# Kernel tuning notes

Hardware: AMD Instinct MI355X
Metric: run time of the kernel (lower is better)

Reference implementation:

```python
import jax, jax.numpy as jnp
import numpy as np

H_HEADS = 16
DECAY_C = 0.7408182206817179  # math.exp(-0.3)


def _gelu(x):
    return jax.nn.gelu(x, approximate=False)  # torch nn.GELU default = exact erf


def _mlp(x, W1, b1, W2, b2):
    return _gelu(x @ W1 + b1) @ W2 + b2


def setup_inputs():
    B, T, C = 4, 2048, 1024
    L = max(64, C // 8)      # lora_dim = 128
    E = int(C * 1.2)         # expanded_dim = 1228
    key = jax.random.key(0)
    ctr = [0]
    def rn(shape, s=0.02):
        ctr[0] += 1
        return jax.random.normal(jax.random.fold_in(key, ctr[0]), shape, jnp.float32) * s
    z = lambda *s: jnp.zeros(s, jnp.float32)
    inp = {
        "queries": rn((B, T, C), 1.0),
        "keys": rn((B, T, C), 1.0),
        "values": rn((B, T, C), 1.0),
        "attn_mask": jnp.ones((B, T), dtype=bool),
        "mu_r": rn((C,)), "mu_k": rn((C,)), "mu_v": rn((C,)),
        "mu_g": rn((C,)), "mu_a": rn((C,)), "mu_d": rn((C,)),
        "dA": rn((C, L)), "dB": rn((L, C)), "db": z(C),
        "aA": rn((C, L)), "aB": rn((L, C)), "ab": z(C),
        "gA": rn((C, L)), "gB": rn((L, C)),
        "rW1": rn((C, E)), "rb1": z(E), "rW2": rn((E, C)), "rb2": z(C),
        "kW1": rn((C, E)), "kb1": z(E), "kW2": rn((E, C)), "kb2": z(C),
        "vW1": rn((C, E)), "vb1": z(E), "vW2": rn((E, C)), "vb2": z(C),
        "oW1": rn((C, E)), "ob1": z(E), "oW2": rn((E, C)), "ob2": z(C),
        "rem_mult": rn((C,), 0.05),
        "iclr_mix": jnp.full((C,), 0.7, jnp.float32),
        "bonus_mult": jnp.full((C,), 1.2, jnp.float32),
        "ln_g": jnp.ones((C,), jnp.float32), "ln_b": z(C),
    }
    return inp


def _forward(queries, mu_r, mu_k, mu_v, mu_g, mu_a, mu_d,
             dA, dB, db, aA, aB, ab, gA, gB,
             rW1, rb1, rW2, rb2, kW1, kb1, kW2, kb2,
             vW1, vb1, vW2, vb2, oW1, ob1, oW2, ob2,
             rem_mult, iclr_mix, bonus_mult, ln_g, ln_b):
    B, T, C = queries.shape
    H = H_HEADS
    N = C // H
    r = _mlp(queries + mu_r, rW1, rb1, rW2, rb2)
    k = _mlp(queries + mu_k, kW1, kb1, kW2, kb2)
    v = _mlp(queries + mu_v, vW1, vb1, vW2, vb2)
    gate = jax.nn.sigmoid(((queries + mu_g) @ gA) @ gB)
    iclr = jax.nn.sigmoid(((queries + mu_a) @ aA) @ ab + ((queries + mu_a) @ aA) @ aB) if False else jax.nn.sigmoid(((queries + mu_a) @ aA) @ aB + ab)
    decay = jnp.exp(-DECAY_C * jax.nn.sigmoid(jnp.tanh(((queries + mu_d) @ dA) @ dB + db)))
    removal_k = k * rem_mult
    replacement_k = k * (1.0 + (iclr - 1.0) * iclr_mix)  # lerp(ones, iclr, mix)
    rh = r.reshape(B, T, H, N)
    rkh = replacement_k.reshape(B, T, H, N)
    vh = v.reshape(B, T, H, N)
    dh = decay.reshape(B, T, H, N)
    ah = iclr.reshape(B, T, H, N)
    rmh = removal_k.reshape(B, T, H, N)
    kn = rmh / jnp.maximum(jnp.linalg.norm(rmh, axis=-1, keepdims=True), 1e-12)  # F.normalize
    # Sequential matrix-state recurrence. G_t = diag(d) - kn (a*kn)^T, so
    # G_t @ S = d[:,None]*S - kn[:,None] * ((a*kn) @ S)  -- rank-1, O(N^2)/step.
    xs = tuple(jnp.swapaxes(a, 0, 1) for a in (dh, ah, kn, rkh, vh, rh))  # [T,B,H,N]
    def step(wkv, x):
        d, a, knt, rk, vt, rt = x
        tmp = jnp.einsum('bhj,bhjk->bhk', a * knt, wkv)
        wkv = d[..., None] * wkv - knt[..., None] * tmp[:, :, None, :] \
              + vt[..., None] * rk[:, :, None, :]
        return wkv, jnp.einsum('bhij,bhj->bhi', wkv, rt)
    wkv0 = jnp.zeros((B, H, N, N), queries.dtype)
    _, out_t = jax.lax.scan(step, wkv0, xs)
    out = jnp.swapaxes(out_t, 0, 1)  # [B,T,H,N]
    bonus = (jnp.sum(rh * rkh, -1, keepdims=True) * 0.2) * vh * bonus_mult.reshape(1, 1, H, N)
    out = (out + bonus).reshape(B, T, C)
    mu = jnp.mean(out, -1, keepdims=True)
    var = jnp.mean((out - mu) ** 2, -1, keepdims=True)
    out = (out - mu) / jnp.sqrt(var + 1e-6) * ln_g + ln_b  # ln_x, eps=1e-6
    out = out * gate
    out = _mlp(out, oW1, ob1, oW2, ob2)  # W_output; dropout is identity in eval
    return out


def reference(queries, keys, values, attn_mask,
              mu_r, mu_k, mu_v, mu_g, mu_a, mu_d,
              dA, dB, db, aA, aB, ab, gA, gB,
              rW1, rb1, rW2, rb2, kW1, kb1, kW2, kb2,
              vW1, vb1, vW2, vb2, oW1, ob1, oW2, ob2,
              rem_mult, iclr_mix, bonus_mult, ln_g, ln_b):
    del keys, values, attn_mask  # accepted but unused by the module's forward
    return _forward(queries, mu_r, mu_k, mu_v, mu_g, mu_a, mu_d,
                    dA, dB, db, aA, aB, ab, gA, gB,
                    rW1, rb1, rW2, rb2, kW1, kb1, kW2, kb2,
                    vW1, vb1, vW2, vb2, oW1, ob1, oW2, ob2,
                    rem_mult, iclr_mix, bonus_mult, ln_g, ln_b)
```

## Files before the change

### kernel.cpp

```cpp
#include <hip/hip_runtime.h>
#include <hip/hip_bf16.h>
#include <math.h>


#define BB 4
#define TT 2048
#define CC 1024
#define HH 16
#define NN 64
#define LL 128
#define EE 1228
#define EPAD 1280
#define MM (BB*TT)
#define TCH 32
#define NSEG 4
#define WARMCH 2
#define DECAY_C_F 0.7408182206817179f

typedef __attribute__((ext_vector_type(8))) short s16x8;
typedef __attribute__((ext_vector_type(4))) float f32x4;

#define GLOAD_LDS16(gp, lp) \
    __builtin_amdgcn_global_load_lds((const __attribute__((address_space(1))) void*)(gp), \
                                     (__attribute__((address_space(3))) void*)(lp), 16, 0, 0)

__global__ __launch_bounds__(256) void fold_pass1_z(
    const float* __restrict__ mu0, const float* __restrict__ mu1, const float* __restrict__ mu2,
    const float* __restrict__ W0,  const float* __restrict__ W1_, const float* __restrict__ W2_,
    float* __restrict__ partial, int ldW, int E, int ldP, int pslice) {
    const float* mu = blockIdx.z == 0 ? mu0 : (blockIdx.z == 1 ? mu1 : mu2);
    const float* W  = blockIdx.z == 0 ? W0  : (blockIdx.z == 1 ? W1_ : W2_);
    partial += (size_t)blockIdx.z * pslice;
    const int l = threadIdx.x & 63;
    const int e = blockIdx.x * 64 + l;
    const int pg = threadIdx.x >> 6;
    const int c0 = blockIdx.y * 64;
    float s = 0.f;
    if (e < E)
        for (int c = c0 + pg; c < c0 + 64; c += 4) s += mu[c] * W[(size_t)c * ldW + e];
    __shared__ float red[4][64];
    red[pg][l] = s;
    __syncthreads();
    if (pg == 0 && e < E)
        partial[(size_t)blockIdx.y * ldP + e] = red[0][l] + red[1][l] + red[2][l] + red[3][l];
}

__global__ void fold_pass2_z(const float* __restrict__ partial,
                             const float* b0, const float* b1, const float* b2,
                             float* __restrict__ outv,
                             int P, int ldP, int pslice, int E, int Epad, int oslice) {
    const float* bias = blockIdx.z == 0 ? b0 : (blockIdx.z == 1 ? b1 : b2);
    partial += (size_t)blockIdx.z * pslice;
    outv    += (size_t)blockIdx.z * oslice;
    int e = blockIdx.x * blockDim.x + threadIdx.x;
    if (e >= Epad) return;
    float s = 0.f;
    if (e < E) {
        s = bias ? bias[e] : 0.f;
        for (int p = 0; p < P; ++p) s += partial[(size_t)p * ldP + e];
    }
    outv[e] = s;
}

__global__ void cast_f32_bf16(const float* __restrict__ in, __hip_bfloat16* __restrict__ out, int n4) {
    int i = blockIdx.x * blockDim.x + threadIdx.x;
    if (i >= n4) return;
    float4 v = ((const float4*)in)[i];
    __hip_bfloat16 o[4] = {__float2bfloat16(v.x), __float2bfloat16(v.y),
                           __float2bfloat16(v.z), __float2bfloat16(v.w)};
    *(ulong1*)&out[i * 4] = *(ulong1*)o;
}

__global__ void transpose_cast_z(const float* s0, const float* s1, const float* s2, const float* s3,
                                 __hip_bfloat16* __restrict__ outT, size_t dslice,
                                 int Rin, int Cin, int Rpad, int Cpad) {
    const float* in = blockIdx.z == 0 ? s0 : (blockIdx.z == 1 ? s1 : (blockIdx.z == 2 ? s2 : s3));
    outT += (size_t)blockIdx.z * dslice;
    __shared__ float t[32][33];
    const int r0 = blockIdx.x * 32, c0 = blockIdx.y * 32;
    const int tx = threadIdx.x, ty = threadIdx.y;
    #pragma unroll
    for (int j = 0; j < 4; ++j) {
        int r = r0 + ty + j * 8, c = c0 + tx;
        t[ty + j * 8][tx] = (r < Rin && c < Cin) ? in[(size_t)r * Cin + c] : 0.f;
    }
    __syncthreads();
    #pragma unroll
    for (int j = 0; j < 4; ++j) {
        int c = c0 + ty + j * 8, r = r0 + tx;
        if (c < Cpad && r < Rpad) outT[(size_t)c * Rpad + r] = __float2bfloat16(t[tx][ty + j * 8]);
    }
}

template<int ACT, int ACTZ2, int OBF, int PADZ>
__global__ __launch_bounds__(256) void gemm_mfma(const __hip_bfloat16* __restrict__ A,
                                                 const __hip_bfloat16* __restrict__ Bt,
                                                 const float* __restrict__ bias,
                                                 void* __restrict__ Cptr,
                                                 int M, int N, int K,
                                                 int ldA, int ldB, int ldC,
                                                 size_t zA, size_t zB, size_t zBias, size_t zC) {
    __shared__ __hip_bfloat16 As[128 * 64];
    __shared__ __hip_bfloat16 Bs[128 * 64];
    const int tid = threadIdx.x;
    const int wid = tid >> 6, lane = tid & 63;
    const int wm = wid >> 1, wn = wid & 1;
    const int bm = blockIdx.y * 128, bn = blockIdx.x * 128;
    A  += (size_t)blockIdx.z * zA;
    Bt += (size_t)blockIdx.z * zB;
    if (bias) bias += (size_t)blockIdx.z * zBias;
    const size_t zc = (size_t)blockIdx.z * zC;
    const int act = (ACTZ2 >= 0 && blockIdx.z == 2) ? ACTZ2 : ACT;

    const __hip_bfloat16* srcA[4];
    const __hip_bfloat16* srcB[4];
    #pragma unroll
    for (int i = 0; i < 4; ++i) {
        int off = (wid * 4 + i) * 1024 + lane * 16;
        int r = off >> 7;
        int c = (off >> 4) & 7;
        int cs = c ^ (r & 7);
        srcA[i] = A  + (size_t)(bm + r) * ldA + cs * 8;
        srcB[i] = Bt + (size_t)(bn + r) * ldB + cs * 8;
    }

    f32x4 acc[4][4];
    #pragma unroll
    for (int i = 0; i < 4; ++i)
        #pragma unroll
        for (int j = 0; j < 4; ++j) acc[i][j] = (f32x4){0.f, 0.f, 0.f, 0.f};

    const int ra = wm * 64 + (lane & 15);
    const int rb = wn * 64 + (lane & 15);

    for (int k0 = 0; k0 < K; k0 += 64) {
        #pragma unroll
        for (int i = 0; i < 4; ++i) {
            GLOAD_LDS16(srcA[i] + k0, (char*)As + (wid * 4 + i) * 1024);
            GLOAD_LDS16(srcB[i] + k0, (char*)Bs + (wid * 4 + i) * 1024);
        }
        __syncthreads();
        #pragma unroll
        for (int h = 0; h < 2; ++h) {
            s16x8 af[4], bfr[4];
            const int kc = (lane >> 4) + h * 4;
            #pragma unroll
            for (int mi = 0; mi < 4; ++mi) {
                int r = ra + mi * 16;
                af[mi] = *(const s16x8*)((const char*)As + r * 128 + (kc ^ (r & 7)) * 16);
            }
            #pragma unroll
            for (int ni = 0; ni < 4; ++ni) {
                int r = rb + ni * 16;
                bfr[ni] = *(const s16x8*)((const char*)Bs + r * 128 + (kc ^ (r & 7)) * 16);
            }
            #pragma unroll
            for (int mi = 0; mi < 4; ++mi)
                #pragma unroll
                for (int ni = 0; ni < 4; ++ni)
                    acc[mi][ni] = __builtin_amdgcn_mfma_f32_16x16x32_bf16(af[mi], bfr[ni], acc[mi][ni], 0, 0, 0);
        }
        __syncthreads();
    }

    #pragma unroll
    for (int ni = 0; ni < 4; ++ni) {
        const int col = bn + wn * 64 + ni * 16 + (lane & 15);
        const bool valid = (col < N);
        const float bc = (valid && bias) ? bias[col] : 0.f;
        #pragma unroll
        for (int mi = 0; mi < 4; ++mi) {
            #pragma unroll
            for (int reg = 0; reg < 4; ++reg) {
                const int row = bm + wm * 64 + mi * 16 + (lane >> 4) * 4 + reg;
                float y = 0.f;
                if (valid) {
                    float x = acc[mi][ni][reg] + bc;
                    if (act == 1)      y = 0.5f * x * (1.0f + erff(x * 0.7071067811865475f));
                    else if (act == 2) y = 1.0f / (1.0f + expf(-x));
                    else if (act == 3) { float sg = 1.0f / (1.0f + expf(-tanhf(x))); y = expf(-DECAY_C_F * sg); }
                    else               y = x;
                }
                if (valid || PADZ) {
                    if (OBF) ((__hip_bfloat16*)Cptr)[zc + (size_t)row * ldC + col] = __float2bfloat16(y);
                    else     ((float*)Cptr)[zc + (size_t)row * ldC + col] = y;
                }
            }
        }
    }
}

#define P_T0(i,j)   pool[0     + (i)*68 + (j)]
#define P_WT(i,j)   pool[4352  + (i)*68 + (j)]
#define P_KP(i,j)   pool[6528  + (i)*68 + (j)]
#define P_P2t(i,j)  pool[6528  + (i)*36 + (j)]
#define P_NU(i,j)   pool[8704  + (i)*68 + (j)]
#define P_GRt(i,j)  pool[8704  + (i)*36 + (j)]
#define P_RKM(i,j)  pool[10880 + (i)*68 + (j)]
#define P_RRM(i,j)  pool[13056 + (i)*68 + (j)]
#define P_GM(i,j)   pool[15232 + (i)*68 + (j)]
#define P_KPT(i,j)  pool[19712 + (i)*36 + (j)]
#define P_NUT(i,j)  pool[22016 + (i)*36 + (j)]
#define P_DCT(i,j)  pool[26624 + (i)*36 + (j)]
#define P_AT(i,j)   pool[28928 + (i)*36 + (j)]
#define P_BM(i,j)   pool[30080 + (i)*36 + (j)]
#define P_SEG(i,j)  pool[31232 + (i)*64 + (j)]
#define LD4(expr)   (*(const float4*)&(expr))
#define FMA4(acc, s, v) { (acc).x = fmaf((s), (v).x, (acc).x); (acc).y = fmaf((s), (v).y, (acc).y); \
                          (acc).z = fmaf((s), (v).z, (acc).z); (acc).w = fmaf((s), (v).w, (acc).w); }
#define DOT4(a, b) ((a).x*(b).x + (a).y*(b).y + (a).z*(b).z + (a).w*(b).w)

__global__ __launch_bounds__(512) void recurrence_chunked(
    const float* __restrict__ kbuf, const __hip_bfloat16* __restrict__ iclr,
    const __hip_bfloat16* __restrict__ dbuf, const float* __restrict__ vbuf,
    const float* __restrict__ rbuf,
    const float* __restrict__ rem_mult, const float* __restrict__ iclr_mix,
    const float* __restrict__ bonus_mult, float* __restrict__ outb) {
    __shared__ float pool[31488];
    const int bh = blockIdx.x & 63, seg = blockIdx.x >> 6;
    const int b = bh >> 4, h = bh & 15;
    const int tid = threadIdx.x, lane = tid & 63, wid = tid >> 6;
    const size_t gbase = ((size_t)b * TT) * CC + (size_t)h * NN;

    for (int i = tid; i < 4352; i += 512) pool[i] = 0.f;
    const int c0 = tid & 63;
    const float remc = rem_mult[h * NN + c0];
    const float mixc = iclr_mix[h * NN + c0];
    __syncthreads();

    const int cout0 = (seg == 0) ? 0 : (seg == 1) ? 18 : (seg == 2) ? 34 : 49;
    const int lenq  = (seg == 0) ? 18 : (seg == 1) ? 16 : 15;
    const int ce    = cout0 + lenq;
    const int cb    = (seg == 0) ? 0 : cout0 - WARMCH;

    for (int chk = cb; chk < ce; ++chk) {
        const bool emit = (chk >= cout0);
        const int tg0 = chk * TCH;
        #pragma unroll
        for (int i = 0; i < 4; ++i) {
            int idx = tid + 512 * i;
            int t = idx >> 6, c = idx & 63;
            size_t off = gbase + (size_t)(tg0 + t) * CC + c;
            float kx = kbuf[off];
            float ax = __bfloat162float(iclr[off]);
            float rk = kx * (1.f + (ax - 1.f) * mixc);
            P_WT(t, c) = ax;
            P_KP(t, c) = kx * remc;
            P_RKM(t, c) = rk;
            P_NU(t, c) = vbuf[off];
            if (emit) P_RRM(t, c) = rbuf[off];
            P_DCT(c, t) = __bfloat162float(dbuf[off]);
        }
        __syncthreads();
        #pragma unroll
        for (int rr = 0; rr < 4; ++rr) {
            int t = wid + rr * 8;
            float v = P_KP(t, lane);
            float ss = v * v;
            #pragma unroll
            for (int s = 32; s; s >>= 1) ss += __shfl_xor(ss, s);
            float kn = v / fmaxf(sqrtf(ss), 1e-12f);
            P_KP(t, lane) = kn;
            P_WT(t, lane) = P_WT(t, lane) * kn;
        }
        float lc[8];
        const int ccs = tid & 63, sgm = tid >> 6, t0s = (sgm & 3) * 8;
        if (tid < 256) {
            float pp_ = 1.f;
            #pragma unroll
            for (int j = 0; j < 8; ++j) { pp_ *= P_DCT(ccs, t0s + j); lc[j] = pp_; }
            P_SEG(sgm, ccs) = pp_;
        }
        __syncthreads();
        if (tid < 256) {
            float m = 1.f;
            for (int s = 0; s < sgm; ++s) m *= P_SEG(s, ccs);
            float dcprev = m;
            #pragma unroll
            for (int j = 0; j < 8; ++j) {
                int t = t0s + j;
                float dcur = m * lc[j];
                P_WT(t, ccs) *= dcprev;
                float inv = 1.f / dcur;
                float kap = P_KP(t, ccs) * inv; P_KP(t, ccs) = kap; P_KPT(ccs, t) = kap;
                float nu  = P_NU(t, ccs) * inv; P_NU(t, ccs) = nu;  P_NUT(ccs, t) = nu;
                P_DCT(ccs, t) = dcur;
                dcprev = dcur;
            }
        }
        __syncthreads();
        #pragma unroll
        for (int u = 0; u < 2; ++u) {
            const int at = wid * 2 + u;
            const int s = (at >> 2) * 8 + (lane >> 3), t = (at & 3) * 8 + (lane & 7);
            float acc = 0.f;
            #pragma unroll
            for (int kc = 0; kc < 16; ++kc) {
                float4 a = LD4(P_KP(s, kc * 4));
                float4 bb = LD4(P_WT(t, kc * 4));
                acc += DOT4(a, bb);
            }
            P_AT(s, t) = (s < t) ? acc : 0.f;
        }
        #pragma unroll
        for (int u = 0; u < 2; ++u) {
            const int bt = wid * 2 + u;
            const int t = (bt >> 2) * 8 + (lane >> 3), s = (bt & 3) * 8 + (lane & 7);
            float acc = 0.f;
            #pragma unroll
            for (int kc = 0; kc < 16; ++kc) {
                float4 a = LD4(P_WT(t, kc * 4));
                float4 bb = LD4(P_NU(s, kc * 4));
                acc += DOT4(a, bb);
            }
            P_BM(t, s) = (s < t) ? acc : 0.f;
        }
        {
            const int t = wid * 4 + (lane >> 4);
            const int q4 = (lane & 15) * 4;
            float4 acc = {0.f, 0.f, 0.f, 0.f};
            #pragma unroll
            for (int j4 = 0; j4 < 16; ++j4) {
                float4 w4 = LD4(P_WT(t, j4 * 4));
                float4 ta = LD4(P_T0(j4 * 4 + 0, q4));
                float4 tb = LD4(P_T0(j4 * 4 + 1, q4));
                float4 tc = LD4(P_T0(j4 * 4 + 2, q4));
                float4 td = LD4(P_T0(j4 * 4 + 3, q4));
                FMA4(acc, w4.x, ta); FMA4(acc, w4.y, tb);
                FMA4(acc, w4.z, tc); FMA4(acc, w4.w, td);
            }
            *(float4*)&P_GM(t, q4) = acc;
        }
        __syncthreads();
        {
            const int t = wid * 4 + (lane >> 4);
            const int q4 = (lane & 15) * 4;
            float4 acc = {0.f, 0.f, 0.f, 0.f};
            #pragma unroll
            for (int s4 = 0; s4 < 8; ++s4) {
                float4 bm4 = LD4(P_BM(t, s4 * 4));
                float4 ra = LD4(P_RKM(s4 * 4 + 0, q4));
                float4 rb = LD4(P_RKM(s4 * 4 + 1, q4));
                float4 rc = LD4(P_RKM(s4 * 4 + 2, q4));
                float4 rd = LD4(P_RKM(s4 * 4 + 3, q4));
                FMA4(acc, bm4.x, ra); FMA4(acc, bm4.y, rb);
                FMA4(acc, bm4.z, rc); FMA4(acc, bm4.w, rd);
            }
            float4 g = LD4(P_GM(t, q4));
            g.x += acc.x; g.y += acc.y; g.z += acc.z; g.w += acc.w;
            *(float4*)&P_GM(t, q4) = g;
        }
        __syncthreads();
        if (wid == 0) {
            float g[32];
            #pragma unroll
            for (int t = 0; t < 32; ++t) g[t] = P_GM(t, lane);
            #pragma unroll
            for (int s = 0; s < 31; ++s) {
                #pragma unroll
                for (int t = s + 1; t < 32; ++t) g[t] -= P_AT(s, t) * g[s];
            }
            #pragma unroll
            for (int t = 0; t < 32; ++t) P_GM(t, lane) = g[t];
        } else if (emit) {
            for (int tile = wid - 1; tile < 16; tile += 7) {
                int t = (tile >> 2) * 8 + (lane >> 3), s = (tile & 3) * 8 + (lane & 7);
                float acc = 0.f;
                #pragma unroll
                for (int kc = 0; kc < 16; ++kc) {
                    float4 a = LD4(P_RRM(t, kc * 4));
                    float4 bb = LD4(P_RKM(s, kc * 4));
                    acc += DOT4(a, bb);
                }
                P_P2t(t, s) = (s <= t) ? acc : 0.f;
            }
        }
        __syncthreads();
        if (emit) {
            for (int tile = wid; tile < 16; tile += 8) {
                int t = (tile >> 2) * 8 + (lane >> 3), s = (tile & 3) * 8 + (lane & 7);
                float acc = 0.f;
                #pragma unroll
                for (int kc = 0; kc < 16; ++kc) {
                    float4 a = LD4(P_RRM(t, kc * 4));
                    float4 bb = LD4(P_GM(s, kc * 4));
                    acc += DOT4(a, bb);
                }
                P_GRt(t, s) = (s <= t) ? acc : 0.f;
            }
            __syncthreads();
            for (int tile = wid; tile < 32; tile += 8) {
                int i = (tile >> 2) * 8 + (lane >> 3), t = (tile & 3) * 8 + (lane & 7);
                float a1 = 0.f, a2 = 0.f, a3 = 0.f;
                #pragma unroll
                for (int j4 = 0; j4 < 16; ++j4) {
                    float4 a = LD4(P_T0(i, j4 * 4));
                    float4 bb = LD4(P_RRM(t, j4 * 4));
                    a1 += DOT4(a, bb);
                }
                #pragma unroll
                for (int s4 = 0; s4 < 8; ++s4) {
                    float4 a = LD4(P_NUT(i, s4 * 4));
                    float4 bb = LD4(P_P2t(t, s4 * 4));
                    a2 += DOT4(a, bb);
                    float4 c = LD4(P_KPT(i, s4 * 4));
                    float4 d = LD4(P_GRt(t, s4 * 4));
                    a3 += DOT4(c, d);
                }
                float diag = 0.2f * bonus_mult[h * NN + i] * P_NUT(i, t) * P_P2t(t, t);
                outb[gbase + (size_t)(tg0 + t) * CC + i] = P_DCT(i, t) * (a1 + a2 + diag - a3);
            }
            __syncthreads();
        }
        #pragma unroll
        for (int u = 0; u < 2; ++u) {
            const int m = wid * 2 + u;
            const int pr = (m & 7) * 8 + (lane >> 3);
            const int q4 = (m >> 3) * 32 + (lane & 7) * 4;
            float4 a1 = {0.f, 0.f, 0.f, 0.f}, a2 = {0.f, 0.f, 0.f, 0.f};
            #pragma unroll
            for (int s = 0; s < 32; ++s) {
                const float kp = P_KPT(pr, s);
                const float nu = P_NUT(pr, s);
                float4 g4 = LD4(P_GM(s, q4));
                float4 rk4 = LD4(P_RKM(s, q4));
                FMA4(a1, kp, g4);
                FMA4(a2, nu, rk4);
            }
            const float dc = P_DCT(pr, 31);
            float4 t0 = LD4(P_T0(pr, q4));
            t0.x = dc * (t0.x - a1.x + a2.x);
            t0.y = dc * (t0.y - a1.y + a2.y);
            t0.z = dc * (t0.z - a1.z + a2.z);
            t0.w = dc * (t0.w - a1.w + a2.w);
            *(float4*)&P_T0(pr, q4) = t0;
        }
        __syncthreads();
    }
}

__global__ __launch_bounds__(256) void ln_gate_kernel(const float* __restrict__ x,
                                                      const __hip_bfloat16* __restrict__ gate,
                                                      const float* __restrict__ g,
                                                      const float* __restrict__ bv,
                                                      __hip_bfloat16* __restrict__ y) {
    const int row = blockIdx.x;
    const float* xr = x + (size_t)row * CC;
    float v[4];
    float s = 0.f;
    #pragma unroll
    for (int j = 0; j < 4; ++j) { v[j] = xr[threadIdx.x + 256 * j]; s += v[j]; }
    __shared__ float red[4], red2[4];
    #pragma unroll
    for (int o = 32; o; o >>= 1) s += __shfl_xor(s, o);
    if ((threadIdx.x & 63) == 0) red[threadIdx.x >> 6] = s;
    __syncthreads();
    const float mean = (red[0] + red[1] + red[2] + red[3]) * (1.f / CC);
    float vs = 0.f;
    #pragma unroll
    for (int j = 0; j < 4; ++j) { float d = v[j] - mean; vs += d * d; }
    #pragma unroll
    for (int o = 32; o; o >>= 1) vs += __shfl_xor(vs, o);
    if ((threadIdx.x & 63) == 0) red2[threadIdx.x >> 6] = vs;
    __syncthreads();
    const float var = (red2[0] + red2[1] + red2[2] + red2[3]) * (1.f / CC);
    const float rstd = rsqrtf(var + 1e-6f);
    #pragma unroll
    for (int j = 0; j < 4; ++j) {
        const int cc = threadIdx.x + 256 * j;
        float o_ = (v[j] - mean) * rstd * g[cc] + bv[cc];
        float gt = __bfloat162float(gate[(size_t)row * CC + cc]);
        y[(size_t)row * CC + cc] = __float2bfloat16(o_ * gt);
    }
}

extern "C" void kernel_launch(void* const* d_in, const int* in_sizes, int n_in,
                              void* d_out, int out_size, void* d_ws, size_t ws_size,
                              hipStream_t stream) {
    const float* q        = (const float*)d_in[0];
    const float* mu_r     = (const float*)d_in[4];
    const float* mu_k     = (const float*)d_in[5];
    const float* mu_v     = (const float*)d_in[6];
    const float* mu_g     = (const float*)d_in[7];
    const float* mu_a     = (const float*)d_in[8];
    const float* mu_d     = (const float*)d_in[9];
    const float* dA       = (const float*)d_in[10];
    const float* dB       = (const float*)d_in[11];
    const float* db       = (const float*)d_in[12];
    const float* aA       = (const float*)d_in[13];
    const float* aB       = (const float*)d_in[14];
    const float* ab       = (const float*)d_in[15];
    const float* gA       = (const float*)d_in[16];
    const float* gB       = (const float*)d_in[17];
    const float* rW1      = (const float*)d_in[18];
    const float* rb1      = (const float*)d_in[19];
    const float* rW2      = (const float*)d_in[20];
    const float* rb2      = (const float*)d_in[21];
    const float* kW1      = (const float*)d_in[22];
    const float* kb1      = (const float*)d_in[23];
    const float* kW2      = (const float*)d_in[24];
    const float* kb2      = (const float*)d_in[25];
    const float* vW1      = (const float*)d_in[26];
    const float* vb1      = (const float*)d_in[27];
    const float* vW2      = (const float*)d_in[28];
    const float* vb2      = (const float*)d_in[29];
    const float* oW1      = (const float*)d_in[30];
    const float* ob1      = (const float*)d_in[31];
    const float* oW2      = (const float*)d_in[32];
    const float* ob2      = (const float*)d_in[33];
    const float* rem_mult = (const float*)d_in[34];
    const float* iclr_mix = (const float*)d_in[35];
    const float* bonus_mult = (const float*)d_in[36];
    const float* ln_g     = (const float*)d_in[37];
    const float* ln_b     = (const float*)d_in[38];
    float* out = (float*)d_out;

    char* p = (char*)d_ws;
    auto alloc = [&](size_t bytes) { char* r = p; p += (bytes + 255) & ~(size_t)255; return r; };
    float* fb_all  = (float*)alloc((size_t)3 * EPAD * 4);
    float* c2_all  = (float*)alloc((size_t)3 * CC * 4);
    float* lt_all  = (float*)alloc((size_t)3 * LL * 4);
    float* cb2_all = (float*)alloc((size_t)3 * CC * 4);
    __hip_bfloat16* qb      = (__hip_bfloat16*)alloc((size_t)MM * CC * 2);
    __hip_bfloat16* W1T_all = (__hip_bfloat16*)alloc((size_t)4 * EPAD * CC * 2);
    __hip_bfloat16* W2T_all = (__hip_bfloat16*)alloc((size_t)4 * CC * EPAD * 2);
    __hip_bfloat16* Hb      = (__hip_bfloat16*)alloc((size_t)MM * 3 * EPAD * 2);
    float*          rkv     = (float*)alloc((size_t)3 * MM * CC * 4);
    __hip_bfloat16* gadbuf  = (__hip_bfloat16*)alloc((size_t)3 * MM * CC * 2);
    __hip_bfloat16* gbuf = gadbuf;
    __hip_bfloat16* abuf = gadbuf + (size_t)MM * CC;
    __hip_bfloat16* dbuf = gadbuf + (size_t)2 * MM * CC;
    float* rbuf = rkv;
    float* kbuf = rkv + (size_t)MM * CC;
    float* vbuf = rkv + (size_t)2 * MM * CC;
    float*          pp      = rkv;
    __hip_bfloat16* AT_all  = (__hip_bfloat16*)((char*)rkv + (1 << 18));
    __hip_bfloat16* BT_all  = (__hip_bfloat16*)((char*)rkv + (1 << 18) + 786432);
    __hip_bfloat16* oW1T    = W1T_all + (size_t)3 * EPAD * CC;
    __hip_bfloat16* oW2T    = W2T_all + (size_t)3 * CC * EPAD;
    __hip_bfloat16* tgad    = Hb;

    const dim3 blk(256);
    const dim3 tblk(32, 8);

    hipMemcpyAsync(cb2_all,          rb2, CC * 4, hipMemcpyDeviceToDevice, stream);
    hipMemcpyAsync(cb2_all + CC,     kb2, CC * 4, hipMemcpyDeviceToDevice, stream);
    hipMemcpyAsync(cb2_all + 2 * CC, vb2, CC * 4, hipMemcpyDeviceToDevice, stream);

    fold_pass1_z<<<dim3(20, 16, 3), blk, 0, stream>>>(mu_r, mu_k, mu_v, rW1, kW1, vW1,
                                                      pp, EE, EE, EPAD, 16 * EPAD);
    fold_pass2_z<<<dim3(5, 1, 3), blk, 0, stream>>>(pp, rb1, kb1, vb1, fb_all,
                                                    16, EPAD, 16 * EPAD, EE, EPAD, EPAD);
    fold_pass1_z<<<dim3(2, 16, 3), blk, 0, stream>>>(mu_g, mu_a, mu_d, gA, aA, dA,
                                                     pp, LL, LL, EPAD, 16 * EPAD);
    fold_pass2_z<<<dim3(1, 1, 3), dim3(128), 0, stream>>>(pp, nullptr, nullptr, nullptr, lt_all,
                                                          16, EPAD, 16 * EPAD, LL, LL, LL);
    fold_pass1_z<<<dim3(16, 2, 3), blk, 0, stream>>>(lt_all, lt_all + LL, lt_all + 2 * LL, gB, aB, dB,
                                                     pp, CC, CC, EPAD, 16 * EPAD);
    fold_pass2_z<<<dim3(4, 1, 3), blk, 0, stream>>>(pp, nullptr, ab, db, c2_all,
                                                    2, EPAD, 16 * EPAD, CC, CC, CC);

    transpose_cast_z<<<dim3(32, 40, 4), tblk, 0, stream>>>(rW1, kW1, vW1, oW1, W1T_all,
                                                           (size_t)EPAD * CC, CC, EE, CC, EPAD);
    transpose_cast_z<<<dim3(40, 32, 4), tblk, 0, stream>>>(rW2, kW2, vW2, oW2, W2T_all,
                                                           (size_t)CC * EPAD, EE, CC, EPAD, CC);
    transpose_cast_z<<<dim3(32, 4, 3), tblk, 0, stream>>>(gA, aA, dA, nullptr, AT_all,
                                                          (size_t)LL * CC, CC, LL, CC, LL);
    transpose_cast_z<<<dim3(4, 32, 3), tblk, 0, stream>>>(gB, aB, dB, nullptr, BT_all,
                                                          (size_t)CC * LL, LL, CC, LL, CC);

    cast_f32_bf16<<<dim3(MM * CC / 4 / 256), blk, 0, stream>>>(q, qb, MM * CC / 4);

    gemm_mfma<0,-1,1,0><<<dim3(3, 64, 1), blk, 0, stream>>>(qb, AT_all, nullptr, tgad,
                                                            MM, 384, CC, CC, CC, 384, 0, 0, 0, 0);
    gemm_mfma<2,3,1,0><<<dim3(8, 64, 3), blk, 0, stream>>>(tgad, BT_all, c2_all, gadbuf,
                                                           MM, CC, LL, 384, LL, CC,
                                                           LL, (size_t)CC * LL, CC, (size_t)MM * CC);

    gemm_mfma<1,-1,1,0><<<dim3(30, 64, 1), blk, 0, stream>>>(qb, W1T_all, fb_all, Hb,
                                                             MM, 3 * EPAD, CC, CC, CC, 3 * EPAD, 0, 0, 0, 0);
    gemm_mfma<0,-1,0,0><<<dim3(8, 64, 3), blk, 0, stream>>>(Hb, W2T_all, cb2_all, rkv,
                                                            MM, CC, EPAD, 3 * EPAD, EPAD, CC,
                                                            EPAD, (size_t)CC * EPAD, CC, (size_t)MM * CC);

    recurrence_chunked<<<dim3(BB * HH * NSEG), dim3(512), 0, stream>>>(
        kbuf, abuf, dbuf, vbuf, rbuf, rem_mult, iclr_mix, bonus_mult, out);

    ln_gate_kernel<<<dim3(MM), blk, 0, stream>>>(out, gbuf, ln_g, ln_b, qb);

    gemm_mfma<1,-1,1,1><<<dim3(10, 64, 1), blk, 0, stream>>>(qb, oW1T, ob1, Hb,
                                                             MM, EE, CC, CC, CC, EPAD, 0, 0, 0, 0);
    gemm_mfma<0,-1,0,0><<<dim3(8, 64, 1), blk, 0, stream>>>(Hb, oW2T, ob2, out,
                                                            MM, CC, EPAD, EPAD, EPAD, CC, 0, 0, 0, 0);
}
```

Measured before the change: 914.1 us.

## Merge LoRA and MLP first/second-stage GEMMs into two combined launches

After: 930.7 us. Within noise of the previous version (+1.8%).

```diff
diff --git a/kernel.cpp b/kernel.cpp
--- a/kernel.cpp
+++ b/kernel.cpp
@@ -15,6 +15,9 @@
 #define TCH 32
 #define NSEG 4
 #define WARMCH 2
+#define N1MEGA 3840
+#define NMEGA  4224
+#define LDH    4224
 #define DECAY_C_F 0.7408182206817179f
 
 typedef __attribute__((ext_vector_type(8))) short s16x8;
@@ -23,6 +26,53 @@
 #define GLOAD_LDS16(gp, lp) \
     __builtin_amdgcn_global_load_lds((const __attribute__((address_space(1))) void*)(gp), \
                                      (__attribute__((address_space(3))) void*)(lp), 16, 0, 0)
+
+__global__ __launch_bounds__(256) void fold_pass1_z6(
+    const float* m0, const float* m1, const float* m2,
+    const float* m3, const float* m4, const float* m5,
+    const float* W0, const float* W1_, const float* W2_,
+    const float* W3, const float* W4, const float* W5,
+    float* __restrict__ partial, int ld0, int E0, int ld1, int E1, int ldP, int pslice) {
+    const int z = blockIdx.z;
+    const float* mu = z == 0 ? m0 : z == 1 ? m1 : z == 2 ? m2 : z == 3 ? m3 : z == 4 ? m4 : m5;
+    const float* W  = z == 0 ? W0 : z == 1 ? W1_ : z == 2 ? W2_ : z == 3 ? W3 : z == 4 ? W4 : W5;
+    const int ldW = (z < 3) ? ld0 : ld1;
+    const int E   = (z < 3) ? E0  : E1;
+    partial += (size_t)z * pslice;
+    const int l = threadIdx.x & 63;
+    const int e = blockIdx.x * 64 + l;
+    const int pg = threadIdx.x >> 6;
+    const int c0 = blockIdx.y * 64;
+    float s = 0.f;
+    if (e < E)
+        for (int c = c0 + pg; c < c0 + 64; c += 4) s += mu[c] * W[(size_t)c * ldW + e];
+    __shared__ float red[4][64];
+    red[pg][l] = s;
+    __syncthreads();
+    if (pg == 0 && e < E)
+        partial[(size_t)blockIdx.y * ldP + e] = red[0][l] + red[1][l] + red[2][l] + red[3][l];
+}
+
+__global__ void fold_pass2_z6(const float* __restrict__ partial,
+                              const float* b0, const float* b1, const float* b2,
+                              float* __restrict__ out0, float* __restrict__ out1,
+                              int P, int ldP, int pslice,
+                              int E0, int Epad0, int osl0, int E1, int Epad1, int osl1) {
+    const int z = blockIdx.z;
+    const float* bias = (z == 0) ? b0 : (z == 1) ? b1 : (z == 2) ? b2 : nullptr;
+    const int E    = (z < 3) ? E0 : E1;
+    const int Epad = (z < 3) ? Epad0 : Epad1;
+    float* outv = (z < 3) ? out0 + (size_t)z * osl0 : out1 + (size_t)(z - 3) * osl1;
+    partial += (size_t)z * pslice;
+    int e = blockIdx.x * blockDim.x + threadIdx.x;
+    if (e >= Epad) return;
+    float s = 0.f;
+    if (e < E) {
+        s = bias ? bias[e] : 0.f;
+        for (int p = 0; p < P; ++p) s += partial[(size_t)p * ldP + e];
+    }
+    outv[e] = s;
+}
 
 __global__ __launch_bounds__(256) void fold_pass1_z(
     const float* __restrict__ mu0, const float* __restrict__ mu1, const float* __restrict__ mu2,
@@ -92,6 +142,200 @@
     }
 }
 
+__device__ __forceinline__ float gemm_act(int act, float x) {
+    if (act == 1)      return 0.5f * x * (1.0f + erff(x * 0.7071067811865475f));
+    else if (act == 2) return 1.0f / (1.0f + expf(-x));
+    else if (act == 3) { float sg = 1.0f / (1.0f + expf(-tanhf(x))); return expf(-DECAY_C_F * sg); }
+    return x;
+}
+
+__global__ __launch_bounds__(256) void gemm_s1(const __hip_bfloat16* __restrict__ A,
+                                               const __hip_bfloat16* __restrict__ Bt,
+                                               const __hip_bfloat16* __restrict__ Bt2,
+                                               const float* __restrict__ bias,
+                                               __hip_bfloat16* __restrict__ Cptr) {
+    __shared__ __hip_bfloat16 As[128 * 64];
+    __shared__ __hip_bfloat16 Bs[128 * 64];
+    const int tid = threadIdx.x;
+    const int wid = tid >> 6, lane = tid & 63;
+    const int wm = wid >> 1, wn = wid & 1;
+    const int bm = blockIdx.y * 128, bn = blockIdx.x * 128;
+    const int K = CC, ldA = CC, ldB = CC, ldC = LDH;
+    const bool mlpBlk = (bn < N1MEGA);
+    const __hip_bfloat16* Bbase = mlpBlk ? (Bt + (size_t)bn * ldB) : (Bt2 + (size_t)(bn - N1MEGA) * ldB);
+
+    const __hip_bfloat16* srcA[4];
+    const __hip_bfloat16* srcB[4];
+    #pragma unroll
+    for (int i = 0; i < 4; ++i) {
+        int off = (wid * 4 + i) * 1024 + lane * 16;
+        int r = off >> 7;
+        int c = (off >> 4) & 7;
+        int cs = c ^ (r & 7);
+        srcA[i] = A + (size_t)(bm + r) * ldA + cs * 8;
+        srcB[i] = Bbase + (size_t)r * ldB + cs * 8;
+    }
+
+    f32x4 acc[4][4];
+    #pragma unroll
+    for (int i = 0; i < 4; ++i)
+        #pragma unroll
+        for (int j = 0; j < 4; ++j) acc[i][j] = (f32x4){0.f, 0.f, 0.f, 0.f};
+
+    const int ra = wm * 64 + (lane & 15);
+    const int rb = wn * 64 + (lane & 15);
+
+    for (int k0 = 0; k0 < K; k0 += 64) {
+        #pragma unroll
+        for (int i = 0; i < 4; ++i) {
+            GLOAD_LDS16(srcA[i] + k0, (char*)As + (wid * 4 + i) * 1024);
+            GLOAD_LDS16(srcB[i] + k0, (char*)Bs + (wid * 4 + i) * 1024);
+        }
+        __syncthreads();
+        #pragma unroll
+        for (int h = 0; h < 2; ++h) {
+            s16x8 af[4], bfr[4];
+            const int kc = (lane >> 4) + h * 4;
+            #pragma unroll
+            for (int mi = 0; mi < 4; ++mi) {
+                int r = ra + mi * 16;
+                af[mi] = *(const s16x8*)((const char*)As + r * 128 + (kc ^ (r & 7)) * 16);
+            }
+            #pragma unroll
+            for (int ni = 0; ni < 4; ++ni) {
+                int r = rb + ni * 16;
+                bfr[ni] = *(const s16x8*)((const char*)Bs + r * 128 + (kc ^ (r & 7)) * 16);
+            }
+            #pragma unroll
+            for (int mi = 0; mi < 4; ++mi)
+                #pragma unroll
+                for (int ni = 0; ni < 4; ++ni)
+                    acc[mi][ni] = __builtin_amdgcn_mfma_f32_16x16x32_bf16(af[mi], bfr[ni], acc[mi][ni], 0, 0, 0);
+        }
+        __syncthreads();
+    }
+
+    #pragma unroll
+    for (int ni = 0; ni < 4; ++ni) {
+        const int col = bn + wn * 64 + ni * 16 + (lane & 15);
+        const float bc = mlpBlk ? bias[col] : 0.f;
+        #pragma unroll
+        for (int mi = 0; mi < 4; ++mi) {
+            #pragma unroll
+            for (int reg = 0; reg < 4; ++reg) {
+                const int row = bm + wm * 64 + mi * 16 + (lane >> 4) * 4 + reg;
+                float x = acc[mi][ni][reg] + bc;
+                float y = mlpBlk ? gemm_act(1, x) : x;
+                Cptr[(size_t)row * ldC + col] = __float2bfloat16(y);
+            }
+        }
+    }
+}
+
+__global__ __launch_bounds__(256) void gemm_s2(const __hip_bfloat16* __restrict__ Hb,
+                                               const __hip_bfloat16* __restrict__ W2T,
+                                               const __hip_bfloat16* __restrict__ BT,
+                                               const float* __restrict__ cb2,
+                                               const float* __restrict__ c2,
+                                               float* __restrict__ rkvout,
+                                               __hip_bfloat16* __restrict__ gadout) {
+    __shared__ __hip_bfloat16 As[128 * 64];
+    __shared__ __hip_bfloat16 Bs[128 * 64];
+    const int tid = threadIdx.x;
+    const int wid = tid >> 6, lane = tid & 63;
+    const int wm = wid >> 1, wn = wid & 1;
+    const int bm = blockIdx.y * 128, bn = blockIdx.x * 128;
+    const int z = blockIdx.z;
+    const int ldA = LDH, ldC = CC;
+
+    const __hip_bfloat16* Asrc;
+    const __hip_bfloat16* Btz;
+    const float* biasz;
+    int K, ldB, act;
+    if (z < 3) {
+        Asrc = Hb + z * EPAD;
+        Btz  = W2T + (size_t)z * CC * EPAD;
+        biasz = cb2 + z * CC;
+        K = EPAD; ldB = EPAD; act = 0;
+    } else {
+        const int w = z - 3;
+        Asrc = Hb + N1MEGA + w * LL;
+        Btz  = BT + (size_t)w * CC * LL;
+        biasz = c2 + w * CC;
+        K = LL; ldB = LL; act = (w == 2) ? 3 : 2;
+    }
+
+    const __hip_bfloat16* srcA[4];
+    const __hip_bfloat16* srcB[4];
+    #pragma unroll
+    for (int i = 0; i < 4; ++i) {
+        int off = (wid * 4 + i) * 1024 + lane * 16;
+        int r = off >> 7;
+        int c = (off >> 4) & 7;
+        int cs = c ^ (r & 7);
+        srcA[i] = Asrc + (size_t)(bm + r) * ldA + cs * 8;
+        srcB[i] = Btz + (size_t)(bn + r) * ldB + cs * 8;
+    }
+
+    f32x4 acc[4][4];
+    #pragma unroll
+    for (int i = 0; i < 4; ++i)
+        #pragma unroll
+        for (int j = 0; j < 4; ++j) acc[i][j] = (f32x4){0.f, 0.f, 0.f, 0.f};
+
+    const int ra = wm * 64 + (lane & 15);
+    const int rb = wn * 64 + (lane & 15);
+
+    for (int k0 = 0; k0 < K; k0 += 64) {
+        #pragma unroll
+        for (int i = 0; i < 4; ++i) {
+            GLOAD_LDS16(srcA[i] + k0, (char*)As + (wid * 4 + i) * 1024);
+            GLOAD_LDS16(srcB[i] + k0, (char*)Bs + (wid * 4 + i) * 1024);
+        }
+        __syncthreads();
+        #pragma unroll
+        for (int h = 0; h < 2; ++h) {
+            s16x8 af[4], bfr[4];
+            const int kc = (lane >> 4) + h * 4;
+            #pragma unroll
+            for (int mi = 0; mi < 4; ++mi) {
+                int r = ra + mi * 16;
+                af[mi] = *(const s16x8*)((const char*)As + r * 128 + (kc ^ (r & 7)) * 16);
+            }
+            #pragma unroll
+            for (int ni = 0; ni < 4; ++ni) {
+                int r = rb + ni * 16;
+                bfr[ni] = *(const s16x8*)((const char*)Bs + r * 128 + (kc ^ (r & 7)) * 16);
+            }
+            #pragma unroll
+            for (int mi = 0; mi < 4; ++mi)
+                #pragma unroll
+                for (int ni = 0; ni < 4; ++ni)
+                    acc[mi][ni] = __builtin_amdgcn_mfma_f32_16x16x32_bf16(af[mi], bfr[ni], acc[mi][ni], 0, 0, 0);
+        }
+        __syncthreads();
+    }
+
+    float* Cf = (z < 3) ? rkvout + (size_t)z * MM * CC : nullptr;
+    __hip_bfloat16* Cb = (z < 3) ? nullptr : gadout + (size_t)(z - 3) * MM * CC;
+
+    #pragma unroll
+    for (int ni = 0; ni < 4; ++ni) {
+        const int col = bn + wn * 64 + ni * 16 + (lane & 15);
+        const float bc = biasz[col];
+        #pragma unroll
+        for (int mi = 0; mi < 4; ++mi) {
+            #pragma unroll
+            for (int reg = 0; reg < 4; ++reg) {
+                const int row = bm + wm * 64 + mi * 16 + (lane >> 4) * 4 + reg;
+                float y = gemm_act(act, acc[mi][ni][reg] + bc);
+                if (Cf) Cf[(size_t)row * ldC + col] = y;
+                else    Cb[(size_t)row * ldC + col] = __float2bfloat16(y);
+            }
+        }
+    }
+}
+
 template<int ACT, int ACTZ2, int OBF, int PADZ>
 __global__ __launch_bounds__(256) void gemm_mfma(const __hip_bfloat16* __restrict__ A,
                                                  const __hip_bfloat16* __restrict__ Bt,
@@ -174,13 +418,7 @@
             for (int reg = 0; reg < 4; ++reg) {
                 const int row = bm + wm * 64 + mi * 16 + (lane >> 4) * 4 + reg;
                 float y = 0.f;
-                if (valid) {
-                    float x = acc[mi][ni][reg] + bc;
-                    if (act == 1)      y = 0.5f * x * (1.0f + erff(x * 0.7071067811865475f));
-                    else if (act == 2) y = 1.0f / (1.0f + expf(-x));
-                    else if (act == 3) { float sg = 1.0f / (1.0f + expf(-tanhf(x))); y = expf(-DECAY_C_F * sg); }
-                    else               y = x;
-                }
+                if (valid) y = gemm_act(act, acc[mi][ni][reg] + bc);
                 if (valid || PADZ) {
                     if (OBF) ((__hip_bfloat16*)Cptr)[zc + (size_t)row * ldC + col] = __float2bfloat16(y);
                     else     ((float*)Cptr)[zc + (size_t)row * ldC + col] = y;
@@ -524,7 +762,9 @@
     __hip_bfloat16* qb      = (__hip_bfloat16*)alloc((size_t)MM * CC * 2);
     __hip_bfloat16* W1T_all = (__hip_bfloat16*)alloc((size_t)4 * EPAD * CC * 2);
     __hip_bfloat16* W2T_all = (__hip_bfloat16*)alloc((size_t)4 * CC * EPAD * 2);
-    __hip_bfloat16* Hb      = (__hip_bfloat16*)alloc((size_t)MM * 3 * EPAD * 2);
+    __hip_bfloat16* AT_all  = (__hip_bfloat16*)alloc((size_t)3 * LL * CC * 2);
+    __hip_bfloat16* BT_all  = (__hip_bfloat16*)alloc((size_t)3 * CC * LL * 2);
+    __hip_bfloat16* Hb      = (__hip_bfloat16*)alloc((size_t)MM * LDH * 2);
     float*          rkv     = (float*)alloc((size_t)3 * MM * CC * 4);
     __hip_bfloat16* gadbuf  = (__hip_bfloat16*)alloc((size_t)3 * MM * CC * 2);
     __hip_bfloat16* gbuf = gadbuf;
@@ -533,12 +773,9 @@
     float* rbuf = rkv;
     float* kbuf = rkv + (size_t)MM * CC;
     float* vbuf = rkv + (size_t)2 * MM * CC;
-    float*          pp      = rkv;
-    __hip_bfloat16* AT_all  = (__hip_bfloat16*)((char*)rkv + (1 << 18));
-    __hip_bfloat16* BT_all  = (__hip_bfloat16*)((char*)rkv + (1 << 18) + 786432);
-    __hip_bfloat16* oW1T    = W1T_all + (size_t)3 * EPAD * CC;
-    __hip_bfloat16* oW2T    = W2T_all + (size_t)3 * CC * EPAD;
-    __hip_bfloat16* tgad    = Hb;
+    float* pp   = rkv;
+    __hip_bfloat16* oW1T = W1T_all + (size_t)3 * EPAD * CC;
+    __hip_bfloat16* oW2T = W2T_all + (size_t)3 * CC * EPAD;
 
     const dim3 blk(256);
     const dim3 tblk(32, 8);
@@ -547,14 +784,13 @@
     hipMemcpyAsync(cb2_all + CC,     kb2, CC * 4, hipMemcpyDeviceToDevice, stream);
     hipMemcpyAsync(cb2_all + 2 * CC, vb2, CC * 4, hipMemcpyDeviceToDevice, stream);
 
-    fold_pass1_z<<<dim3(20, 16, 3), blk, 0, stream>>>(mu_r, mu_k, mu_v, rW1, kW1, vW1,
-                                                      pp, EE, EE, EPAD, 16 * EPAD);
-    fold_pass2_z<<<dim3(5, 1, 3), blk, 0, stream>>>(pp, rb1, kb1, vb1, fb_all,
-                                                    16, EPAD, 16 * EPAD, EE, EPAD, EPAD);
-    fold_pass1_z<<<dim3(2, 16, 3), blk, 0, stream>>>(mu_g, mu_a, mu_d, gA, aA, dA,
-                                                     pp, LL, LL, EPAD, 16 * EPAD);
-    fold_pass2_z<<<dim3(1, 1, 3), dim3(128), 0, stream>>>(pp, nullptr, nullptr, nullptr, lt_all,
-                                                          16, EPAD, 16 * EPAD, LL, LL, LL);
+    fold_pass1_z6<<<dim3(20, 16, 6), blk, 0, stream>>>(
+        mu_r, mu_k, mu_v, mu_g, mu_a, mu_d,
+        rW1, kW1, vW1, gA, aA, dA,
+        pp, EE, EE, LL, LL, EPAD, 16 * EPAD);
+    fold_pass2_z6<<<dim3(5, 1, 6), blk, 0, stream>>>(
+        pp, rb1, kb1, vb1, fb_all, lt_all,
+        16, EPAD, 16 * EPAD, EE, EPAD, EPAD, LL, LL, LL);
     fold_pass1_z<<<dim3(16, 2, 3), blk, 0, stream>>>(lt_all, lt_all + LL, lt_all + 2 * LL, gB, aB, dB,
                                                      pp, CC, CC, EPAD, 16 * EPAD);
     fold_pass2_z<<<dim3(4, 1, 3), blk, 0, stream>>>(pp, nullptr, ab, db, c2_all,
@@ -571,17 +807,10 @@
 
     cast_f32_bf16<<<dim3(MM * CC / 4 / 256), blk, 0, stream>>>(q, qb, MM * CC / 4);
 
-    gemm_mfma<0,-1,1,0><<<dim3(3, 64, 1), blk, 0, stream>>>(qb, AT_all, nullptr, tgad,
-                                                            MM, 384, CC, CC, CC, 384, 0, 0, 0, 0);
-    gemm_mfma<2,3,1,0><<<dim3(8, 64, 3), blk, 0, stream>>>(tgad, BT_all, c2_all, gadbuf,
-                                                           MM, CC, LL, 384, LL, CC,
-                                                           LL, (size_t)CC * LL, CC, (size_t)MM * CC);
-
-    gemm_mfma<1,-1,1,0><<<dim3(30, 64, 1), blk, 0, stream>>>(qb, W1T_all, fb_all, Hb,
-                                                             MM, 3 * EPAD, CC, CC, CC, 3 * EPAD, 0, 0, 0, 0);
-    gemm_mfma<0,-1,0,0><<<dim3(8, 64, 3), blk, 0, stream>>>(Hb, W2T_all, cb2_all, rkv,
-                                                            MM, CC, EPAD, 3 * EPAD, EPAD, CC,
-                                                            EPAD, (size_t)CC * EPAD, CC, (size_t)MM * CC);
+    gemm_s1<<<dim3(NMEGA / 128, MM / 128), blk, 0, stream>>>(qb, W1T_all, AT_all, fb_all, Hb);
+
+    gemm_s2<<<dim3(CC / 128, MM / 128, 6), blk, 0, stream>>>(Hb, W2T_all, BT_all,
+                                                             cb2_all, c2_all, rkv, gadbuf);
 
     recurrence_chunked<<<dim3(BB * HH * NSEG), dim3(512), 0, stream>>>(
         kbuf, abuf, dbuf, vbuf, rbuf, rem_mult, iclr_mix, bonus_mult, out);
```
